# Performance work log

Measured on AMD Instinct MI355X. Metric: run time of the kernel, lower is better.

## Reference

```python
import jax, jax.numpy as jnp
import numpy as np
import math


def setup_inputs() -> dict:
    key = jax.random.key(0)
    kq, kk, kv = jax.random.split(key, 3)
    B, HQ, HKV, S, D = 1, 32, 8, 2048, 128
    query = jax.random.normal(kq, (B, HQ, S, D), dtype=jnp.float32)
    key_s = jax.random.normal(kk, (B, HKV, S, D), dtype=jnp.float32)
    value = jax.random.normal(kv, (B, HKV, S, D), dtype=jnp.float32)
    # additive causal mask [B,1,S,S]: 0 where j<=i, large-negative elsewhere
    neg = jnp.finfo(jnp.float32).min
    i = jnp.arange(S)
    attention_mask = jnp.where(i[None, :] <= i[:, None], 0.0, neg).astype(jnp.float32)[None, None]
    return {"query": query, "key": key_s, "value": value,
            "attention_mask": attention_mask, "window_size": 1024}


def reference(query, key, value, attention_mask, window_size):
    B, HQ, S, D = query.shape
    groups = HQ // key.shape[1]
    scaling = 1.0 / math.sqrt(D)
    # repeat_kv (GQA -> MHA)
    k = jnp.repeat(key, groups, axis=1)   # [B,HQ,S,D]
    v = jnp.repeat(value, groups, axis=1)
    # ---- eager_attention_forward ----
    scores = jnp.einsum('bhqd,bhkd->bhqk', query, k) * scaling
    scores = scores + attention_mask[:, :, :, :S]
    attn_weights = jax.nn.softmax(scores.astype(jnp.float32), axis=-1).astype(query.dtype)
    attn_output = jnp.einsum('bhqk,bhkd->bhqd', attn_weights, v)
    attn_output = attn_output.transpose(0, 2, 1, 3)  # [B,S,HQ,D]
    # ---- compute_window_attn_weights ----
    W = window_size
    qw = query[:, :, -W:, :]                                  # [B,HQ,W,D]
    ww = jnp.einsum('bhqd,bhkd->bhqk', qw, k) / math.sqrt(D)  # [B,HQ,W,S]
    neg = jnp.finfo(ww.dtype).min
    r = jnp.arange(W)
    win_mask = jnp.where(r[None, :] <= r[:, None], 0.0, neg).astype(ww.dtype)  # [W,W]
    ww = ww.at[:, :, :, -W:].add(win_mask[None, None])
    window_attn_weights = jax.nn.softmax(ww.astype(jnp.float32), axis=-1).astype(query.dtype)
    return (attn_output, attn_weights, window_attn_weights)
```

## Files before the change

kernel.cpp:

```cpp
#include <hip/hip_runtime.h>
#include <hip/hip_bf16.h>

typedef __bf16 bf16x8 __attribute__((ext_vector_type(8)));
typedef float f32x4 __attribute__((ext_vector_type(4)));
static_assert(sizeof(bf16x8) == 16, "bf16x8 must be 16B");

constexpr int S = 2048, D = 128, HQ = 32, W = 1024;
constexpr float SCALE_L2E = 0.08838834764831845f * 1.4426950408889634f;

constexpr size_t O1 = (size_t)S * HQ * D;
constexpr size_t O2 = O1 + (size_t)HQ * S * S;
constexpr int TILE_BYTES = 64 * 256;

__device__ __forceinline__ void gl_lds16(const void* g, void* l) {
    __builtin_amdgcn_global_load_lds(
        (const __attribute__((address_space(1))) void*)(unsigned long long)g,
        (__attribute__((address_space(3))) void*)(unsigned int)(unsigned long long)l,
        16, 0, 0);
}

__global__ __launch_bounds__(256)
void prep_kernel(const float* __restrict__ K, const float* __restrict__ V,
                 char* __restrict__ KbI, char* __restrict__ VtI)
{
    __shared__ __attribute__((aligned(16))) __bf16 Vs[128][72];
    const int b = blockIdx.x, hkv = b >> 5, kt = b & 31;
    const int tid = threadIdx.x;
    const float* Ks   = K + ((size_t)hkv * S + kt * 64) * D;
    const float* Vsrc = V + ((size_t)hkv * S + kt * 64) * D;
    char* Kimg = KbI + (size_t)(hkv * 32 + kt) * TILE_BYTES;
    char* Vimg = VtI + (size_t)(hkv * 32 + kt) * TILE_BYTES;

    #pragma unroll
    for (int i = 0; i < 4; ++i) {
        int idx = tid + i * 256;
        int r = idx >> 4, sl = idx & 15;
        float4 a = *reinterpret_cast<const float4*>(Ks + r * D + sl * 8);
        float4 c = *reinterpret_cast<const float4*>(Ks + r * D + sl * 8 + 4);
        bf16x8 f = {(__bf16)a.x, (__bf16)a.y, (__bf16)a.z, (__bf16)a.w,
                    (__bf16)c.x, (__bf16)c.y, (__bf16)c.z, (__bf16)c.w};
        *reinterpret_cast<bf16x8*>(Kimg + r * 256 + ((sl * 16) ^ ((r & 7) << 4))) = f;
    }
    #pragma unroll
    for (int i = 0; i < 8; ++i) {
        int idx = tid + i * 256;
        int r = idx >> 5, c = (idx & 31) * 4;
        float4 vv = *reinterpret_cast<const float4*>(Vsrc + r * D + c);
        Vs[c + 0][r] = (__bf16)vv.x; Vs[c + 1][r] = (__bf16)vv.y;
        Vs[c + 2][r] = (__bf16)vv.z; Vs[c + 3][r] = (__bf16)vv.w;
    }
    __syncthreads();
    #pragma unroll
    for (int i = 0; i < 4; ++i) {
        int idx = tid + i * 256;
        int d = idx >> 3, sl = idx & 7;
        bf16x8 v = *reinterpret_cast<const bf16x8*>(&Vs[d][sl * 8]);
        *reinterpret_cast<bf16x8*>(Vimg + d * 128 + ((sl * 16) ^ ((d & 7) << 4))) = v;
    }
}

__global__ __launch_bounds__(256, 2)
void attn_fused2(const float* __restrict__ Q, const char* __restrict__ KbI,
                 const char* __restrict__ VtI, float* __restrict__ out)
{
    __shared__ __attribute__((aligned(16))) char LDS_K[2][TILE_BYTES];
    __shared__ __attribute__((aligned(16))) char LDS_V[2][TILE_BYTES];
    __shared__ __attribute__((aligned(16))) char LDS_P[4][2048];

    const int bid = blockIdx.x;
    const int h   = bid >> 5;
    const int qt  = 31 - (((bid & 31) + h) & 31);
    const int hkv = h >> 2;
    const int q0  = qt << 6;
    const int tid = threadIdx.x, wave = tid >> 6, lane = tid & 63;
    const int lo = lane & 15, hi = lane >> 4;
    const int qw0 = q0 + wave * 16;
    const bool winrows = (q0 >= W);

    const char* Ktiles = KbI + (size_t)hkv * 32 * TILE_BYTES;
    const char* Vtiles = VtI + (size_t)hkv * 32 * TILE_BYTES;
    const float* Qh = Q + (size_t)h * S * D;

    bf16x8 qf[4];
    {
        const float* qs = Qh + (size_t)(qw0 + lo) * D + hi * 8;
        #pragma unroll
        for (int dc = 0; dc < 4; ++dc) {
            float4 a = *reinterpret_cast<const float4*>(qs + dc * 32);
            float4 b = *reinterpret_cast<const float4*>(qs + dc * 32 + 4);
            bf16x8 f;
            f[0] = (__bf16)(a.x * SCALE_L2E); f[1] = (__bf16)(a.y * SCALE_L2E);
            f[2] = (__bf16)(a.z * SCALE_L2E); f[3] = (__bf16)(a.w * SCALE_L2E);
            f[4] = (__bf16)(b.x * SCALE_L2E); f[5] = (__bf16)(b.y * SCALE_L2E);
            f[6] = (__bf16)(b.z * SCALE_L2E); f[7] = (__bf16)(b.w * SCALE_L2E);
            qf[dc] = f;
        }
    }

    #pragma unroll
    for (int i = 0; i < 4; ++i)
        gl_lds16(Ktiles + (wave * 4 + i) * 1024 + lane * 16,
                 LDS_K[0] + (wave * 4 + i) * 1024);
    __builtin_amdgcn_sched_barrier(0);
    asm volatile("s_waitcnt vmcnt(0)" ::: "memory");
    __builtin_amdgcn_s_barrier();
    __builtin_amdgcn_sched_barrier(0);

    float lsum[4] = {0.f, 0.f, 0.f, 0.f};
    int cur = 0;
    for (int kt = 0; kt <= qt; ++kt) {
        if (kt < qt) {
            const char* src = Ktiles + (size_t)(kt + 1) * TILE_BYTES;
            #pragma unroll
            for (int i = 0; i < 4; ++i)
                gl_lds16(src + (wave * 4 + i) * 1024 + lane * 16,
                         LDS_K[cur ^ 1] + (wave * 4 + i) * 1024);
            __builtin_amdgcn_sched_barrier(0);
        }
        const char* KtB = LDS_K[cur];
        #pragma unroll
        for (int cg = 0; cg < 4; ++cg) {
            f32x4 acc = {0.f, 0.f, 0.f, 0.f};
            const int row = cg * 16 + lo, swzr = (row & 7) << 4;
            #pragma unroll
            for (int dc = 0; dc < 4; ++dc) {
                bf16x8 kf = *reinterpret_cast<const bf16x8*>(
                    KtB + row * 256 + ((hi * 16 + dc * 64) ^ swzr));
                acc = __builtin_amdgcn_mfma_f32_16x16x32_bf16(qf[dc], kf, acc, 0, 0, 0);
            }
            const int k = (kt << 6) + cg * 16 + lo;
            #pragma unroll
            for (int r = 0; r < 4; ++r) {
                int q = qw0 + hi * 4 + r;
                lsum[r] += (k <= q) ? exp2f(acc[r]) : 0.f;
            }
        }
        if (kt < qt) {
            asm volatile("s_waitcnt vmcnt(0)" ::: "memory");
            __builtin_amdgcn_s_barrier();
            __builtin_amdgcn_sched_barrier(0);
        }
        cur ^= 1;
    }
    float rcp_[4];
    #pragma unroll
    for (int r = 0; r < 4; ++r) {
        float v = lsum[r];
        v += __shfl_xor(v, 1); v += __shfl_xor(v, 2);
        v += __shfl_xor(v, 4); v += __shfl_xor(v, 8);
        rcp_[r] = 1.0f / v;
    }

    __builtin_amdgcn_s_barrier();
    #pragma unroll
    for (int i = 0; i < 4; ++i) {
        gl_lds16(Ktiles + (wave * 4 + i) * 1024 + lane * 16, LDS_K[0] + (wave * 4 + i) * 1024);
        gl_lds16(Vtiles + (wave * 4 + i) * 1024 + lane * 16, LDS_V[0] + (wave * 4 + i) * 1024);
    }
    __builtin_amdgcn_sched_barrier(0);
    asm volatile("s_waitcnt vmcnt(0)" ::: "memory");
    __builtin_amdgcn_s_barrier();
    __builtin_amdgcn_sched_barrier(0);

    f32x4 oacc[8];
    #pragma unroll
    for (int i = 0; i < 8; ++i) oacc[i] = (f32x4){0.f, 0.f, 0.f, 0.f};
    char* Ps = LDS_P[wave];
    cur = 0;

    for (int kt = 0; kt <= qt; ++kt) {
        if (kt < qt) {
            const char* sk = Ktiles + (size_t)(kt + 1) * TILE_BYTES;
            const char* sv = Vtiles + (size_t)(kt + 1) * TILE_BYTES;
            #pragma unroll
            for (int i = 0; i < 4; ++i) {
                gl_lds16(sk + (wave * 4 + i) * 1024 + lane * 16, LDS_K[cur ^ 1] + (wave * 4 + i) * 1024);
                gl_lds16(sv + (wave * 4 + i) * 1024 + lane * 16, LDS_V[cur ^ 1] + (wave * 4 + i) * 1024);
            }
            __builtin_amdgcn_sched_barrier(0);
        }
        const char* KtB = LDS_K[cur];
        const char* VtB = LDS_V[cur];
        const int kbase = kt << 6;

        #pragma unroll
        for (int cg = 0; cg < 4; ++cg) {
            f32x4 acc = {0.f, 0.f, 0.f, 0.f};
            const int row = cg * 16 + lo, swzr = (row & 7) << 4;
            #pragma unroll
            for (int dc = 0; dc < 4; ++dc) {
                bf16x8 kf = *reinterpret_cast<const bf16x8*>(
                    KtB + row * 256 + ((hi * 16 + dc * 64) ^ swzr));
                acc = __builtin_amdgcn_mfma_f32_16x16x32_bf16(qf[dc], kf, acc, 0, 0, 0);
            }
            const int k = kbase + cg * 16 + lo;
            #pragma unroll
            for (int r = 0; r < 4; ++r) {
                const int q = qw0 + hi * 4 + r;
                float p = (k <= q) ? exp2f(acc[r]) * rcp_[r] : 0.f;
                const int prow = hi * 4 + r;
                *reinterpret_cast<__bf16*>(
                    Ps + prow * 128 + ((2 * (cg * 16 + lo)) ^ ((prow & 7) << 4))) = (__bf16)p;
            }
        }

        {
            const int row = lane >> 2;
            const int q = qw0 + row;
            float* dstP = out + O1 + ((size_t)h * S + q) * S + kbase;
            #pragma unroll
            for (int t = 0; t < 2; ++t) {
                int boff = (((lane & 3) * 16 + t * 64) ^ ((row & 7) << 4));
                bf16x8 pv8 = *reinterpret_cast<const bf16x8*>(Ps + row * 128 + boff);
                float4 f0 = {(float)pv8[0], (float)pv8[1], (float)pv8[2], (float)pv8[3]};
                float4 f1 = {(float)pv8[4], (float)pv8[5], (float)pv8[6], (float)pv8[7]};
                int k0 = (lane & 3) * 8 + t * 32;
                *reinterpret_cast<float4*>(dstP + k0) = f0;
                *reinterpret_cast<float4*>(dstP + k0 + 4) = f1;
                if (winrows) {
                    float* dstW = out + O2 + ((size_t)h * W + (q - W)) * S + kbase;
                    *reinterpret_cast<float4*>(dstW + k0) = f0;
                    *reinterpret_cast<float4*>(dstW + k0 + 4) = f1;
                }
            }
        }

        #pragma unroll
        for (int kc = 0; kc < 2; ++kc) {
            const int cb = (kc * 64 + hi * 16) ^ ((lo & 7) << 4);
            bf16x8 pf = *reinterpret_cast<const bf16x8*>(Ps + lo * 128 + cb);
            #pragma unroll
            for (int dg = 0; dg < 8; ++dg) {
                bf16x8 vf = *reinterpret_cast<const bf16x8*>(VtB + (dg * 16 + lo) * 128 + cb);
                oacc[dg] = __builtin_amdgcn_mfma_f32_16x16x32_bf16(pf, vf, oacc[dg], 0, 0, 0);
            }
        }

        if (kt < qt) {
            asm volatile("s_waitcnt vmcnt(4)" ::: "memory");
            __builtin_amdgcn_s_barrier();
            __builtin_amdgcn_sched_barrier(0);
        }
        cur ^= 1;
    }

    {
        const int r0 = tid >> 4;
        const int c4 = (tid & 15) * 4;
        const float4 z = {0.f, 0.f, 0.f, 0.f};
        for (int kt = qt + 1; kt < 32; ++kt) {
            const int kbase = kt << 6;
            #pragma unroll
            for (int i = 0; i < 4; ++i) {
                const int q = q0 + r0 + i * 16;
                *reinterpret_cast<float4*>(&out[O1 + ((size_t)h * S + q) * S + kbase + c4]) = z;
                if (winrows)
                    *reinterpret_cast<float4*>(&out[O2 + ((size_t)h * W + (q - W)) * S + kbase + c4]) = z;
            }
        }
    }

    #pragma unroll
    for (int dg = 0; dg < 8; ++dg) {
        #pragma unroll
        for (int r = 0; r < 4; ++r) {
            const int q = qw0 + hi * 4 + r;
            out[((size_t)q * HQ + h) * D + dg * 16 + lo] = oacc[dg][r];
        }
    }
}

extern "C" void kernel_launch(void* const* d_in, const int* in_sizes, int n_in,
                              void* d_out, int out_size, void* d_ws, size_t ws_size,
                              hipStream_t stream)
{
    const float* Q = (const float*)d_in[0];
    const float* K = (const float*)d_in[1];
    const float* V = (const float*)d_in[2];
    float* out = (float*)d_out;

    char* KbI = (char*)d_ws;
    char* VtI = (char*)d_ws + (size_t)4 * 1024 * 1024;

    hipLaunchKernelGGL(prep_kernel, dim3(256),  dim3(256), 0, stream, K, V, KbI, VtI);
    hipLaunchKernelGGL(attn_fused2, dim3(1024), dim3(256), 0, stream, Q, KbI, VtI, out);
}
```

Measured before the change: 278.7 us.

## Pair complementary causal query tiles in 512-thread blocks sharing K/V loads

Each block now covers two query tiles (16+p and 15-p) with eight waves, so causal work per block is balanced and each K/V tile loaded into LDS feeds both query tiles. Global-to-LDS loads are split across twice as many waves, and the wait counts now depend on how many loads each wave group issued. Waves whose tile has already finished its causal range sit idle at barriers, and __launch_bounds__(512,4) puts more pressure on registers.

```diff
diff --git a/kernel.cpp b/kernel.cpp
--- a/kernel.cpp
+++ b/kernel.cpp
@@ -59,23 +59,26 @@
     }
 }
 
-__global__ __launch_bounds__(256, 2)
-void attn_fused2(const float* __restrict__ Q, const char* __restrict__ KbI,
+__global__ __launch_bounds__(512, 4)
+void attn_fused3(const float* __restrict__ Q, const char* __restrict__ KbI,
                  const char* __restrict__ VtI, float* __restrict__ out)
 {
     __shared__ __attribute__((aligned(16))) char LDS_K[2][TILE_BYTES];
     __shared__ __attribute__((aligned(16))) char LDS_V[2][TILE_BYTES];
-    __shared__ __attribute__((aligned(16))) char LDS_P[4][2048];
+    __shared__ __attribute__((aligned(16))) char LDS_P[8][2048];
 
     const int bid = blockIdx.x;
-    const int h   = bid >> 5;
-    const int qt  = 31 - (((bid & 31) + h) & 31);
+    const int h   = bid & 31;
+    const int p   = bid >> 5;
+    const int qt1 = 16 + p;
+    const int qt2 = 15 - p;
     const int hkv = h >> 2;
-    const int q0  = qt << 6;
     const int tid = threadIdx.x, wave = tid >> 6, lane = tid & 63;
     const int lo = lane & 15, hi = lane >> 4;
-    const int qw0 = q0 + wave * 16;
-    const bool winrows = (q0 >= W);
+    const int rg   = wave >> 2;
+    const int qt_r = rg ? qt2 : qt1;
+    const int qw0  = (qt_r << 6) + (wave & 3) * 16;
+    const bool winw = (rg == 0);
 
     const char* Ktiles = KbI + (size_t)hkv * 32 * TILE_BYTES;
     const char* Vtiles = VtI + (size_t)hkv * 32 * TILE_BYTES;
@@ -98,9 +101,9 @@
     }
 
     #pragma unroll
-    for (int i = 0; i < 4; ++i)
-        gl_lds16(Ktiles + (wave * 4 + i) * 1024 + lane * 16,
-                 LDS_K[0] + (wave * 4 + i) * 1024);
+    for (int i = 0; i < 2; ++i)
+        gl_lds16(Ktiles + (wave * 2 + i) * 1024 + lane * 16,
+                 LDS_K[0] + (wave * 2 + i) * 1024);
     __builtin_amdgcn_sched_barrier(0);
     asm volatile("s_waitcnt vmcnt(0)" ::: "memory");
     __builtin_amdgcn_s_barrier();
@@ -108,34 +111,36 @@
 
     float lsum[4] = {0.f, 0.f, 0.f, 0.f};
     int cur = 0;
-    for (int kt = 0; kt <= qt; ++kt) {
-        if (kt < qt) {
+    for (int kt = 0; kt <= qt1; ++kt) {
+        if (kt < qt1) {
             const char* src = Ktiles + (size_t)(kt + 1) * TILE_BYTES;
             #pragma unroll
-            for (int i = 0; i < 4; ++i)
-                gl_lds16(src + (wave * 4 + i) * 1024 + lane * 16,
-                         LDS_K[cur ^ 1] + (wave * 4 + i) * 1024);
-            __builtin_amdgcn_sched_barrier(0);
-        }
-        const char* KtB = LDS_K[cur];
-        #pragma unroll
-        for (int cg = 0; cg < 4; ++cg) {
-            f32x4 acc = {0.f, 0.f, 0.f, 0.f};
-            const int row = cg * 16 + lo, swzr = (row & 7) << 4;
-            #pragma unroll
-            for (int dc = 0; dc < 4; ++dc) {
-                bf16x8 kf = *reinterpret_cast<const bf16x8*>(
-                    KtB + row * 256 + ((hi * 16 + dc * 64) ^ swzr));
-                acc = __builtin_amdgcn_mfma_f32_16x16x32_bf16(qf[dc], kf, acc, 0, 0, 0);
-            }
-            const int k = (kt << 6) + cg * 16 + lo;
-            #pragma unroll
-            for (int r = 0; r < 4; ++r) {
-                int q = qw0 + hi * 4 + r;
-                lsum[r] += (k <= q) ? exp2f(acc[r]) : 0.f;
-            }
-        }
-        if (kt < qt) {
+            for (int i = 0; i < 2; ++i)
+                gl_lds16(src + (wave * 2 + i) * 1024 + lane * 16,
+                         LDS_K[cur ^ 1] + (wave * 2 + i) * 1024);
+            __builtin_amdgcn_sched_barrier(0);
+        }
+        if (kt <= qt_r) {
+            const char* KtB = LDS_K[cur];
+            #pragma unroll
+            for (int cg = 0; cg < 4; ++cg) {
+                f32x4 acc = {0.f, 0.f, 0.f, 0.f};
+                const int row = cg * 16 + lo, swzr = (row & 7) << 4;
+                #pragma unroll
+                for (int dc = 0; dc < 4; ++dc) {
+                    bf16x8 kf = *reinterpret_cast<const bf16x8*>(
+                        KtB + row * 256 + ((hi * 16 + dc * 64) ^ swzr));
+                    acc = __builtin_amdgcn_mfma_f32_16x16x32_bf16(qf[dc], kf, acc, 0, 0, 0);
+                }
+                const int k = (kt << 6) + cg * 16 + lo;
+                #pragma unroll
+                for (int r = 0; r < 4; ++r) {
+                    int q = qw0 + hi * 4 + r;
+                    lsum[r] += (k <= q) ? exp2f(acc[r]) : 0.f;
+                }
+            }
+        }
+        if (kt < qt1) {
             asm volatile("s_waitcnt vmcnt(0)" ::: "memory");
             __builtin_amdgcn_s_barrier();
             __builtin_amdgcn_sched_barrier(0);
@@ -153,9 +158,9 @@
 
     __builtin_amdgcn_s_barrier();
     #pragma unroll
-    for (int i = 0; i < 4; ++i) {
-        gl_lds16(Ktiles + (wave * 4 + i) * 1024 + lane * 16, LDS_K[0] + (wave * 4 + i) * 1024);
-        gl_lds16(Vtiles + (wave * 4 + i) * 1024 + lane * 16, LDS_V[0] + (wave * 4 + i) * 1024);
+    for (int i = 0; i < 2; ++i) {
+        gl_lds16(Ktiles + (wave * 2 + i) * 1024 + lane * 16, LDS_K[0] + (wave * 2 + i) * 1024);
+        gl_lds16(Vtiles + (wave * 2 + i) * 1024 + lane * 16, LDS_V[0] + (wave * 2 + i) * 1024);
     }
     __builtin_amdgcn_sched_barrier(0);
     asm volatile("s_waitcnt vmcnt(0)" ::: "memory");
@@ -168,76 +173,79 @@
     char* Ps = LDS_P[wave];
     cur = 0;
 
-    for (int kt = 0; kt <= qt; ++kt) {
-        if (kt < qt) {
+    for (int kt = 0; kt <= qt1; ++kt) {
+        if (kt < qt1) {
             const char* sk = Ktiles + (size_t)(kt + 1) * TILE_BYTES;
             const char* sv = Vtiles + (size_t)(kt + 1) * TILE_BYTES;
             #pragma unroll
-            for (int i = 0; i < 4; ++i) {
-                gl_lds16(sk + (wave * 4 + i) * 1024 + lane * 16, LDS_K[cur ^ 1] + (wave * 4 + i) * 1024);
-                gl_lds16(sv + (wave * 4 + i) * 1024 + lane * 16, LDS_V[cur ^ 1] + (wave * 4 + i) * 1024);
-            }
-            __builtin_amdgcn_sched_barrier(0);
-        }
-        const char* KtB = LDS_K[cur];
-        const char* VtB = LDS_V[cur];
-        const int kbase = kt << 6;
-
-        #pragma unroll
-        for (int cg = 0; cg < 4; ++cg) {
-            f32x4 acc = {0.f, 0.f, 0.f, 0.f};
-            const int row = cg * 16 + lo, swzr = (row & 7) << 4;
-            #pragma unroll
-            for (int dc = 0; dc < 4; ++dc) {
-                bf16x8 kf = *reinterpret_cast<const bf16x8*>(
-                    KtB + row * 256 + ((hi * 16 + dc * 64) ^ swzr));
-                acc = __builtin_amdgcn_mfma_f32_16x16x32_bf16(qf[dc], kf, acc, 0, 0, 0);
-            }
-            const int k = kbase + cg * 16 + lo;
-            #pragma unroll
-            for (int r = 0; r < 4; ++r) {
-                const int q = qw0 + hi * 4 + r;
-                float p = (k <= q) ? exp2f(acc[r]) * rcp_[r] : 0.f;
-                const int prow = hi * 4 + r;
-                *reinterpret_cast<__bf16*>(
-                    Ps + prow * 128 + ((2 * (cg * 16 + lo)) ^ ((prow & 7) << 4))) = (__bf16)p;
-            }
-        }
-
-        {
-            const int row = lane >> 2;
-            const int q = qw0 + row;
-            float* dstP = out + O1 + ((size_t)h * S + q) * S + kbase;
-            #pragma unroll
-            for (int t = 0; t < 2; ++t) {
-                int boff = (((lane & 3) * 16 + t * 64) ^ ((row & 7) << 4));
-                bf16x8 pv8 = *reinterpret_cast<const bf16x8*>(Ps + row * 128 + boff);
-                float4 f0 = {(float)pv8[0], (float)pv8[1], (float)pv8[2], (float)pv8[3]};
-                float4 f1 = {(float)pv8[4], (float)pv8[5], (float)pv8[6], (float)pv8[7]};
-                int k0 = (lane & 3) * 8 + t * 32;
-                *reinterpret_cast<float4*>(dstP + k0) = f0;
-                *reinterpret_cast<float4*>(dstP + k0 + 4) = f1;
-                if (winrows) {
-                    float* dstW = out + O2 + ((size_t)h * W + (q - W)) * S + kbase;
-                    *reinterpret_cast<float4*>(dstW + k0) = f0;
-                    *reinterpret_cast<float4*>(dstW + k0 + 4) = f1;
-                }
-            }
-        }
-
-        #pragma unroll
-        for (int kc = 0; kc < 2; ++kc) {
-            const int cb = (kc * 64 + hi * 16) ^ ((lo & 7) << 4);
-            bf16x8 pf = *reinterpret_cast<const bf16x8*>(Ps + lo * 128 + cb);
-            #pragma unroll
-            for (int dg = 0; dg < 8; ++dg) {
-                bf16x8 vf = *reinterpret_cast<const bf16x8*>(VtB + (dg * 16 + lo) * 128 + cb);
-                oacc[dg] = __builtin_amdgcn_mfma_f32_16x16x32_bf16(pf, vf, oacc[dg], 0, 0, 0);
-            }
-        }
-
-        if (kt < qt) {
-            asm volatile("s_waitcnt vmcnt(4)" ::: "memory");
+            for (int i = 0; i < 2; ++i) {
+                gl_lds16(sk + (wave * 2 + i) * 1024 + lane * 16, LDS_K[cur ^ 1] + (wave * 2 + i) * 1024);
+                gl_lds16(sv + (wave * 2 + i) * 1024 + lane * 16, LDS_V[cur ^ 1] + (wave * 2 + i) * 1024);
+            }
+            __builtin_amdgcn_sched_barrier(0);
+        }
+        if (kt <= qt_r) {
+            const char* KtB = LDS_K[cur];
+            const char* VtB = LDS_V[cur];
+            const int kbase = kt << 6;
+
+            #pragma unroll
+            for (int cg = 0; cg < 4; ++cg) {
+                f32x4 acc = {0.f, 0.f, 0.f, 0.f};
+                const int row = cg * 16 + lo, swzr = (row & 7) << 4;
+                #pragma unroll
+                for (int dc = 0; dc < 4; ++dc) {
+                    bf16x8 kf = *reinterpret_cast<const bf16x8*>(
+                        KtB + row * 256 + ((hi * 16 + dc * 64) ^ swzr));
+                    acc = __builtin_amdgcn_mfma_f32_16x16x32_bf16(qf[dc], kf, acc, 0, 0, 0);
+                }
+                const int k = kbase + cg * 16 + lo;
+                #pragma unroll
+                for (int r = 0; r < 4; ++r) {
+                    const int q = qw0 + hi * 4 + r;
+                    float pv = (k <= q) ? exp2f(acc[r]) * rcp_[r] : 0.f;
+                    const int prow = hi * 4 + r;
+                    *reinterpret_cast<__bf16*>(
+                        Ps + prow * 128 + ((2 * (cg * 16 + lo)) ^ ((prow & 7) << 4))) = (__bf16)pv;
+                }
+            }
+
+            {
+                const int row = lane >> 2;
+                const int q = qw0 + row;
+                float* dstP = out + O1 + ((size_t)h * S + q) * S + kbase;
+                #pragma unroll
+                for (int t = 0; t < 2; ++t) {
+                    int boff = (((lane & 3) * 16 + t * 64) ^ ((row & 7) << 4));
+                    bf16x8 pv8 = *reinterpret_cast<const bf16x8*>(Ps + row * 128 + boff);
+                    float4 f0 = {(float)pv8[0], (float)pv8[1], (float)pv8[2], (float)pv8[3]};
+                    float4 f1 = {(float)pv8[4], (float)pv8[5], (float)pv8[6], (float)pv8[7]};
+                    int k0 = (lane & 3) * 8 + t * 32;
+                    *reinterpret_cast<float4*>(dstP + k0) = f0;
+                    *reinterpret_cast<float4*>(dstP + k0 + 4) = f1;
+                    if (winw) {
+                        float* dstW = out + O2 + ((size_t)h * W + (q - W)) * S + kbase;
+                        *reinterpret_cast<float4*>(dstW + k0) = f0;
+                        *reinterpret_cast<float4*>(dstW + k0 + 4) = f1;
+                    }
+                }
+            }
+
+            #pragma unroll
+            for (int kc = 0; kc < 2; ++kc) {
+                const int cb = (kc * 64 + hi * 16) ^ ((lo & 7) << 4);
+                bf16x8 pf = *reinterpret_cast<const bf16x8*>(Ps + lo * 128 + cb);
+                #pragma unroll
+                for (int dg = 0; dg < 8; ++dg) {
+                    bf16x8 vf = *reinterpret_cast<const bf16x8*>(VtB + (dg * 16 + lo) * 128 + cb);
+                    oacc[dg] = __builtin_amdgcn_mfma_f32_16x16x32_bf16(pf, vf, oacc[dg], 0, 0, 0);
+                }
+            }
+        }
+        if (kt < qt1) {
+            if (rg == 0)            asm volatile("s_waitcnt vmcnt(8)" ::: "memory");
+            else if (kt <= qt2)     asm volatile("s_waitcnt vmcnt(4)" ::: "memory");
+            else                    asm volatile("s_waitcnt vmcnt(0)" ::: "memory");
             __builtin_amdgcn_s_barrier();
             __builtin_amdgcn_sched_barrier(0);
         }
@@ -245,17 +253,18 @@
     }
 
     {
-        const int r0 = tid >> 4;
-        const int c4 = (tid & 15) * 4;
+        const int zr = lane >> 2;
+        const int c0 = (lane & 3) * 16;
         const float4 z = {0.f, 0.f, 0.f, 0.f};
-        for (int kt = qt + 1; kt < 32; ++kt) {
-            const int kbase = kt << 6;
-            #pragma unroll
-            for (int i = 0; i < 4; ++i) {
-                const int q = q0 + r0 + i * 16;
-                *reinterpret_cast<float4*>(&out[O1 + ((size_t)h * S + q) * S + kbase + c4]) = z;
-                if (winrows)
-                    *reinterpret_cast<float4*>(&out[O2 + ((size_t)h * W + (q - W)) * S + kbase + c4]) = z;
+        const int q = qw0 + zr;
+        for (int kt = qt_r + 1; kt < 32; ++kt) {
+            float* dp = out + O1 + ((size_t)h * S + q) * S + kt * 64 + c0;
+            #pragma unroll
+            for (int j = 0; j < 4; ++j) *reinterpret_cast<float4*>(dp + j * 4) = z;
+            if (winw) {
+                float* dw = out + O2 + ((size_t)h * W + (q - W)) * S + kt * 64 + c0;
+                #pragma unroll
+                for (int j = 0; j < 4; ++j) *reinterpret_cast<float4*>(dw + j * 4) = z;
             }
         }
     }
@@ -282,6 +291,6 @@
     char* KbI = (char*)d_ws;
     char* VtI = (char*)d_ws + (size_t)4 * 1024 * 1024;
 
-    hipLaunchKernelGGL(prep_kernel, dim3(256),  dim3(256), 0, stream, K, V, KbI, VtI);
-    hipLaunchKernelGGL(attn_fused2, dim3(1024), dim3(256), 0, stream, Q, KbI, VtI, out);
-}
+    hipLaunchKernelGGL(prep_kernel, dim3(256), dim3(256), 0, stream, K, V, KbI, VtI);
+    hipLaunchKernelGGL(attn_fused3, dim3(512), dim3(512), 0, stream, Q, KbI, VtI, out);
+}
```

After: 263.5 us. 1.06x faster.

## Single-buffer K/V LDS tiles for higher occupancy, remap blocks, use nontemporal stores

Applied to the files above, without the earlier changes.

Replaces the double-buffered K/V LDS tiles with single buffers and raises launch bounds to 4 blocks per CU, so more waves can hide latency in place of software prefetch. Each tile load is now followed by a blocking wait and barrier, so load latency is exposed within a block. Block-to-(head, q-tile) mapping is changed to interleave heavy and light causal tiles and to group heads. All large output writes (probabilities, window weights, zero fill, attention output) switch to nontemporal stores, and the zero fill is re-indexed per wave.

```diff
diff --git a/kernel.cpp b/kernel.cpp
--- a/kernel.cpp
+++ b/kernel.cpp
@@ -17,6 +17,9 @@
         (const __attribute__((address_space(1))) void*)(unsigned long long)g,
         (__attribute__((address_space(3))) void*)(unsigned int)(unsigned long long)l,
         16, 0, 0);
+}
+__device__ __forceinline__ void st_nt4(float* p, f32x4 v) {
+    __builtin_nontemporal_store(v, reinterpret_cast<f32x4*>(p));
 }
 
 __global__ __launch_bounds__(256)
@@ -59,23 +62,25 @@
     }
 }
 
-__global__ __launch_bounds__(256, 2)
-void attn_fused2(const float* __restrict__ Q, const char* __restrict__ KbI,
+__global__ __launch_bounds__(256, 4)
+void attn_fused4(const float* __restrict__ Q, const char* __restrict__ KbI,
                  const char* __restrict__ VtI, float* __restrict__ out)
 {
-    __shared__ __attribute__((aligned(16))) char LDS_K[2][TILE_BYTES];
-    __shared__ __attribute__((aligned(16))) char LDS_V[2][TILE_BYTES];
+    __shared__ __attribute__((aligned(16))) char LDS_K[TILE_BYTES];
+    __shared__ __attribute__((aligned(16))) char LDS_V[TILE_BYTES];
     __shared__ __attribute__((aligned(16))) char LDS_P[4][2048];
 
     const int bid = blockIdx.x;
-    const int h   = bid >> 5;
-    const int qt  = 31 - (((bid & 31) + h) & 31);
+    const int j   = bid >> 5;
+    const int qt = (j < 8) ? (16 + j) : (j < 16) ? (23 - j) : (j < 24) ? (47 - j) : (j - 24);
+    const int b5 = bid & 31;
+    const int h  = (b5 & 7) * 4 + (b5 >> 3);
     const int hkv = h >> 2;
     const int q0  = qt << 6;
     const int tid = threadIdx.x, wave = tid >> 6, lane = tid & 63;
     const int lo = lane & 15, hi = lane >> 4;
     const int qw0 = q0 + wave * 16;
-    const bool winrows = (q0 >= W);
+    const bool winw = (qt >= 16);
 
     const char* Ktiles = KbI + (size_t)hkv * 32 * TILE_BYTES;
     const char* Vtiles = VtI + (size_t)hkv * 32 * TILE_BYTES;
@@ -97,27 +102,17 @@
         }
     }
 
-    #pragma unroll
-    for (int i = 0; i < 4; ++i)
-        gl_lds16(Ktiles + (wave * 4 + i) * 1024 + lane * 16,
-                 LDS_K[0] + (wave * 4 + i) * 1024);
-    __builtin_amdgcn_sched_barrier(0);
-    asm volatile("s_waitcnt vmcnt(0)" ::: "memory");
-    __builtin_amdgcn_s_barrier();
-    __builtin_amdgcn_sched_barrier(0);
-
     float lsum[4] = {0.f, 0.f, 0.f, 0.f};
-    int cur = 0;
     for (int kt = 0; kt <= qt; ++kt) {
-        if (kt < qt) {
-            const char* src = Ktiles + (size_t)(kt + 1) * TILE_BYTES;
-            #pragma unroll
-            for (int i = 0; i < 4; ++i)
-                gl_lds16(src + (wave * 4 + i) * 1024 + lane * 16,
-                         LDS_K[cur ^ 1] + (wave * 4 + i) * 1024);
-            __builtin_amdgcn_sched_barrier(0);
-        }
-        const char* KtB = LDS_K[cur];
+        const char* src = Ktiles + (size_t)kt * TILE_BYTES;
+        #pragma unroll
+        for (int i = 0; i < 4; ++i)
+            gl_lds16(src + (wave * 4 + i) * 1024 + lane * 16,
+                     LDS_K + (wave * 4 + i) * 1024);
+        __builtin_amdgcn_sched_barrier(0);
+        asm volatile("s_waitcnt vmcnt(0)" ::: "memory");
+        __builtin_amdgcn_s_barrier();
+        __builtin_amdgcn_sched_barrier(0);
         #pragma unroll
         for (int cg = 0; cg < 4; ++cg) {
             f32x4 acc = {0.f, 0.f, 0.f, 0.f};
@@ -125,7 +120,7 @@
             #pragma unroll
             for (int dc = 0; dc < 4; ++dc) {
                 bf16x8 kf = *reinterpret_cast<const bf16x8*>(
-                    KtB + row * 256 + ((hi * 16 + dc * 64) ^ swzr));
+                    LDS_K + row * 256 + ((hi * 16 + dc * 64) ^ swzr));
                 acc = __builtin_amdgcn_mfma_f32_16x16x32_bf16(qf[dc], kf, acc, 0, 0, 0);
             }
             const int k = (kt << 6) + cg * 16 + lo;
@@ -135,12 +130,10 @@
                 lsum[r] += (k <= q) ? exp2f(acc[r]) : 0.f;
             }
         }
-        if (kt < qt) {
-            asm volatile("s_waitcnt vmcnt(0)" ::: "memory");
-            __builtin_amdgcn_s_barrier();
-            __builtin_amdgcn_sched_barrier(0);
-        }
-        cur ^= 1;
+        __builtin_amdgcn_sched_barrier(0);
+        asm volatile("s_waitcnt lgkmcnt(0)" ::: "memory");
+        __builtin_amdgcn_s_barrier();
+        __builtin_amdgcn_sched_barrier(0);
     }
     float rcp_[4];
     #pragma unroll
@@ -151,36 +144,24 @@
         rcp_[r] = 1.0f / v;
     }
 
-    __builtin_amdgcn_s_barrier();
-    #pragma unroll
-    for (int i = 0; i < 4; ++i) {
-        gl_lds16(Ktiles + (wave * 4 + i) * 1024 + lane * 16, LDS_K[0] + (wave * 4 + i) * 1024);
-        gl_lds16(Vtiles + (wave * 4 + i) * 1024 + lane * 16, LDS_V[0] + (wave * 4 + i) * 1024);
-    }
-    __builtin_amdgcn_sched_barrier(0);
-    asm volatile("s_waitcnt vmcnt(0)" ::: "memory");
-    __builtin_amdgcn_s_barrier();
-    __builtin_amdgcn_sched_barrier(0);
-
     f32x4 oacc[8];
     #pragma unroll
     for (int i = 0; i < 8; ++i) oacc[i] = (f32x4){0.f, 0.f, 0.f, 0.f};
     char* Ps = LDS_P[wave];
-    cur = 0;
 
     for (int kt = 0; kt <= qt; ++kt) {
-        if (kt < qt) {
-            const char* sk = Ktiles + (size_t)(kt + 1) * TILE_BYTES;
-            const char* sv = Vtiles + (size_t)(kt + 1) * TILE_BYTES;
-            #pragma unroll
-            for (int i = 0; i < 4; ++i) {
-                gl_lds16(sk + (wave * 4 + i) * 1024 + lane * 16, LDS_K[cur ^ 1] + (wave * 4 + i) * 1024);
-                gl_lds16(sv + (wave * 4 + i) * 1024 + lane * 16, LDS_V[cur ^ 1] + (wave * 4 + i) * 1024);
-            }
-            __builtin_amdgcn_sched_barrier(0);
-        }
-        const char* KtB = LDS_K[cur];
-        const char* VtB = LDS_V[cur];
+        const char* sk = Ktiles + (size_t)kt * TILE_BYTES;
+        const char* sv = Vtiles + (size_t)kt * TILE_BYTES;
+        #pragma unroll
+        for (int i = 0; i < 4; ++i) {
+            gl_lds16(sk + (wave * 4 + i) * 1024 + lane * 16, LDS_K + (wave * 4 + i) * 1024);
+            gl_lds16(sv + (wave * 4 + i) * 1024 + lane * 16, LDS_V + (wave * 4 + i) * 1024);
+        }
+        __builtin_amdgcn_sched_barrier(0);
+        asm volatile("s_waitcnt vmcnt(0)" ::: "memory");
+        __builtin_amdgcn_s_barrier();
+        __builtin_amdgcn_sched_barrier(0);
+
         const int kbase = kt << 6;
 
         #pragma unroll
@@ -190,17 +171,17 @@
             #pragma unroll
             for (int dc = 0; dc < 4; ++dc) {
                 bf16x8 kf = *reinterpret_cast<const bf16x8*>(
-                    KtB + row * 256 + ((hi * 16 + dc * 64) ^ swzr));
+                    LDS_K + row * 256 + ((hi * 16 + dc * 64) ^ swzr));
                 acc = __builtin_amdgcn_mfma_f32_16x16x32_bf16(qf[dc], kf, acc, 0, 0, 0);
             }
             const int k = kbase + cg * 16 + lo;
             #pragma unroll
             for (int r = 0; r < 4; ++r) {
                 const int q = qw0 + hi * 4 + r;
-                float p = (k <= q) ? exp2f(acc[r]) * rcp_[r] : 0.f;
+                float pv = (k <= q) ? exp2f(acc[r]) * rcp_[r] : 0.f;
                 const int prow = hi * 4 + r;
                 *reinterpret_cast<__bf16*>(
-                    Ps + prow * 128 + ((2 * (cg * 16 + lo)) ^ ((prow & 7) << 4))) = (__bf16)p;
+                    Ps + prow * 128 + ((2 * (cg * 16 + lo)) ^ ((prow & 7) << 4))) = (__bf16)pv;
             }
         }
 
@@ -212,15 +193,15 @@
             for (int t = 0; t < 2; ++t) {
                 int boff = (((lane & 3) * 16 + t * 64) ^ ((row & 7) << 4));
                 bf16x8 pv8 = *reinterpret_cast<const bf16x8*>(Ps + row * 128 + boff);
-                float4 f0 = {(float)pv8[0], (float)pv8[1], (float)pv8[2], (float)pv8[3]};
-                float4 f1 = {(float)pv8[4], (float)pv8[5], (float)pv8[6], (float)pv8[7]};
+                f32x4 f0 = {(float)pv8[0], (float)pv8[1], (float)pv8[2], (float)pv8[3]};
+                f32x4 f1 = {(float)pv8[4], (float)pv8[5], (float)pv8[6], (float)pv8[7]};
                 int k0 = (lane & 3) * 8 + t * 32;
-                *reinterpret_cast<float4*>(dstP + k0) = f0;
-                *reinterpret_cast<float4*>(dstP + k0 + 4) = f1;
-                if (winrows) {
+                st_nt4(dstP + k0, f0);
+                st_nt4(dstP + k0 + 4, f1);
+                if (winw) {
                     float* dstW = out + O2 + ((size_t)h * W + (q - W)) * S + kbase;
-                    *reinterpret_cast<float4*>(dstW + k0) = f0;
-                    *reinterpret_cast<float4*>(dstW + k0 + 4) = f1;
+                    st_nt4(dstW + k0, f0);
+                    st_nt4(dstW + k0 + 4, f1);
                 }
             }
         }
@@ -231,31 +212,30 @@
             bf16x8 pf = *reinterpret_cast<const bf16x8*>(Ps + lo * 128 + cb);
             #pragma unroll
             for (int dg = 0; dg < 8; ++dg) {
-                bf16x8 vf = *reinterpret_cast<const bf16x8*>(VtB + (dg * 16 + lo) * 128 + cb);
+                bf16x8 vf = *reinterpret_cast<const bf16x8*>(LDS_V + (dg * 16 + lo) * 128 + cb);
                 oacc[dg] = __builtin_amdgcn_mfma_f32_16x16x32_bf16(pf, vf, oacc[dg], 0, 0, 0);
             }
         }
 
-        if (kt < qt) {
-            asm volatile("s_waitcnt vmcnt(4)" ::: "memory");
-            __builtin_amdgcn_s_barrier();
-            __builtin_amdgcn_sched_barrier(0);
-        }
-        cur ^= 1;
+        __builtin_amdgcn_sched_barrier(0);
+        asm volatile("s_waitcnt lgkmcnt(0)" ::: "memory");
+        __builtin_amdgcn_s_barrier();
+        __builtin_amdgcn_sched_barrier(0);
     }
 
     {
-        const int r0 = tid >> 4;
-        const int c4 = (tid & 15) * 4;
-        const float4 z = {0.f, 0.f, 0.f, 0.f};
+        const int zr = lane >> 2;
+        const int c0 = (lane & 3) * 16;
+        const f32x4 z = {0.f, 0.f, 0.f, 0.f};
+        const int q = qw0 + zr;
         for (int kt = qt + 1; kt < 32; ++kt) {
-            const int kbase = kt << 6;
-            #pragma unroll
-            for (int i = 0; i < 4; ++i) {
-                const int q = q0 + r0 + i * 16;
-                *reinterpret_cast<float4*>(&out[O1 + ((size_t)h * S + q) * S + kbase + c4]) = z;
-                if (winrows)
-                    *reinterpret_cast<float4*>(&out[O2 + ((size_t)h * W + (q - W)) * S + kbase + c4]) = z;
+            float* dp = out + O1 + ((size_t)h * S + q) * S + kt * 64 + c0;
+            #pragma unroll
+            for (int jj = 0; jj < 4; ++jj) st_nt4(dp + jj * 4, z);
+            if (winw) {
+                float* dw = out + O2 + ((size_t)h * W + (q - W)) * S + kt * 64 + c0;
+                #pragma unroll
+                for (int jj = 0; jj < 4; ++jj) st_nt4(dw + jj * 4, z);
             }
         }
     }
@@ -265,7 +245,7 @@
         #pragma unroll
         for (int r = 0; r < 4; ++r) {
             const int q = qw0 + hi * 4 + r;
-            out[((size_t)q * HQ + h) * D + dg * 16 + lo] = oacc[dg][r];
+            __builtin_nontemporal_store(oacc[dg][r], out + ((size_t)q * HQ + h) * D + dg * 16 + lo);
         }
     }
 }
@@ -283,5 +263,5 @@
     char* VtI = (char*)d_ws + (size_t)4 * 1024 * 1024;
 
     hipLaunchKernelGGL(prep_kernel, dim3(256),  dim3(256), 0, stream, K, V, KbI, VtI);
-    hipLaunchKernelGGL(attn_fused2, dim3(1024), dim3(256), 0, stream, Q, KbI, VtI, out);
-}
+    hipLaunchKernelGGL(attn_fused4, dim3(1024), dim3(256), 0, stream, Q, KbI, VtI, out);
+}
```

Result: slower. 811.1 us (+191.0%).
